# Kernel optimization log

Measured on AMD Instinct MI355X. Metric: run time of the kernel, lower is better.

## Reference

```python
import jax, jax.numpy as jnp
import numpy as np

B, D, E, K = 8192, 1024, 8, 5  # batch, in_dim, num_size_classes, num_depth_classes
H = max(64, D)                 # hidden = max(64, in_dim)
EPS = 1e-8


def ordinal_logits_to_probs(logits, num_classes):
    # logits: [B, K-1] cumulative ordinal logits -> [B, K] class probs
    q = jax.nn.sigmoid(logits)
    probs = jnp.concatenate(
        [1.0 - q[:, :1], q[:, :-1] - q[:, 1:], q[:, -1:]], axis=1
    )  # [B, K]
    probs = jnp.clip(probs, EPS)
    return probs / jnp.clip(probs.sum(axis=1, keepdims=True), EPS)


def setup_inputs() -> dict:
    key = jax.random.key(0)
    kx, ks, k1, k2 = jax.random.split(key, 4)
    x = jax.random.normal(kx, (B, D), dtype=jnp.float32)
    size_idx = jax.random.randint(ks, (B,), 0, E, dtype=jnp.int64)
    # per-expert 2-layer MLP params: Linear(D,H) -> ReLU -> Linear(H,K-1)
    W1 = jax.random.normal(k1, (E, D, H), dtype=jnp.float32) / np.sqrt(D)
    b1 = jnp.zeros((E, H), dtype=jnp.float32)
    W2 = jax.random.normal(k2, (E, H, K - 1), dtype=jnp.float32) / np.sqrt(H)
    b2 = jnp.zeros((E, K - 1), dtype=jnp.float32)
    return {"x": x, "size_idx": size_idx, "W1": W1, "b1": b1, "W2": W2, "b2": b2}


def reference(x, size_idx, W1, b1, W2, b2):
    # Hard routing: each token gets the output of expert size_idx[b].
    # Dense all-expert compute + per-token select (same math as mask/gather/scatter,
    # dropout is inference-mode identity).
    h = jax.nn.relu(jnp.einsum('bd,edh->beh', x, W1) + b1)      # [B, E, H]
    all_logits = jnp.einsum('beh,ehk->bek', h, W2) + b2          # [B, E, K-1]
    idx = size_idx.astype(jnp.int32)[:, None, None]              # [B, 1, 1]
    logits = jnp.take_along_axis(all_logits, idx, axis=1)[:, 0]  # [B, K-1]
    probs = ordinal_logits_to_probs(logits, K)                   # [B, K]
    return logits, probs
```

## Files before the change

kernel.cpp:

```cpp
#include <hip/hip_runtime.h>
#include <cstdint>
#include <cstddef>

#define Bn 8192
#define Dn 1024
#define Hn 1024
#define En 8
#define MT 128
#define MAX_TILES (Bn / MT + En)
#define PERM_N (Bn + En * MT)

typedef unsigned short u16;
typedef __bf16 bf16x8 __attribute__((ext_vector_type(8)));
typedef float f32x4 __attribute__((ext_vector_type(4)));
typedef unsigned short ushort8 __attribute__((ext_vector_type(8)));

__device__ __forceinline__ u16 f2bf(float f) {
  unsigned int u = __float_as_uint(f);
  unsigned int r = u + 0x7fffu + ((u >> 16) & 1u);
  return (u16)(r >> 16);
}

__device__ __forceinline__ void gld16(const void* g, void* l) {
  __builtin_amdgcn_global_load_lds(
      (const __attribute__((address_space(1))) void*)g,
      (__attribute__((address_space(3))) void*)l, 16, 0, 0);
}

__global__ __launch_bounds__(1024) void route_k(const int* __restrict__ sidx,
                                                int* __restrict__ off,
                                                int* __restrict__ perm) {
  __shared__ int hist[16][En];
  __shared__ int base[16][En];
  __shared__ int eoff[En + 1];
  int t = threadIdx.x;
  int wv = t >> 6;
  if (t < 16 * En) ((int*)hist)[t] = 0;
  __syncthreads();
  int e8[8], r8[8];
#pragma unroll
  for (int i = 0; i < 8; i++) {
    int e = sidx[t + i * 1024];
    e8[i] = e;
    r8[i] = atomicAdd(&hist[wv][e], 1);
  }
  __syncthreads();
  if (t < En) {
    int s = 0;
    for (int w = 0; w < 16; w++) { base[w][t] = s; s += hist[w][t]; }
    hist[0][t] = s;
  }
  __syncthreads();
  if (t == 0) {
    int o = 0;
    for (int e = 0; e < En; e++) {
      eoff[e] = o; off[e] = o;
      o += (hist[0][e] + MT - 1) & ~(MT - 1);
    }
    eoff[En] = o; off[En] = o;
  }
  __syncthreads();
#pragma unroll
  for (int i = 0; i < 8; i++) {
    int e = e8[i];
    perm[eoff[e] + base[wv][e] + r8[i]] = t + i * 1024;
  }
}

__global__ void cvt_x_k(const float* __restrict__ x, u16* __restrict__ xb) {
  size_t i = ((size_t)blockIdx.x * blockDim.x + threadIdx.x) * 8;
  float4 a = *(const float4*)(x + i);
  float4 b = *(const float4*)(x + i + 4);
  ushort8 o;
  o[0] = f2bf(a.x); o[1] = f2bf(a.y); o[2] = f2bf(a.z); o[3] = f2bf(a.w);
  o[4] = f2bf(b.x); o[5] = f2bf(b.y); o[6] = f2bf(b.z); o[7] = f2bf(b.w);
  *(ushort8*)(xb + i) = o;
}

__global__ __launch_bounds__(256) void cvt_w1_k(const float* __restrict__ W1,
                                                u16* __restrict__ W1t) {
  __shared__ float tile[64][65];
  int e = blockIdx.z;
  int k0 = blockIdx.y * 64;
  int n0 = blockIdx.x * 64;
  int c = threadIdx.x & 63, r0 = threadIdx.x >> 6;
  const float* src = W1 + ((size_t)e << 20) + (size_t)k0 * Hn + n0;
#pragma unroll
  for (int i = 0; i < 16; i++) {
    int r = r0 + i * 4;
    tile[r][c] = src[(size_t)r * Hn + c];
  }
  __syncthreads();
  u16* dst = W1t + ((size_t)e << 20) + (size_t)n0 * Dn + k0;
#pragma unroll
  for (int i = 0; i < 16; i++) {
    int h = r0 + i * 4;
    dst[(size_t)h * Dn + c] = f2bf(tile[c][h]);
  }
}

__global__ __launch_bounds__(256) void gemm_k(
    const u16* __restrict__ xb, const u16* __restrict__ w1t,
    const float* __restrict__ b1, const float* __restrict__ w2,
    const int* __restrict__ perm, const int* __restrict__ off,
    float* __restrict__ out) {
  __shared__ u16 As[2][128 * 32];
  __shared__ u16 Bs[2][128 * 32];

  int tb = blockIdx.x;
  int row0 = tb * MT;
  if (row0 >= off[En]) return;
  int e = 0;
  while (row0 >= off[e + 1]) e++;
  int n0 = blockIdx.y * 128;

  int tid = threadIdx.x;
  int lane = tid & 63, w = tid >> 6;
  int wm = w >> 1, wn = w & 1;

  int srow = lane >> 2;
  int slot = lane & 3;
  int q = slot ^ ((srow >> 1) & 3);
  int scol = q * 8;
  const u16* aG[2]; const u16* bG[2];
  u16* aL[2]; u16* bL[2];
#pragma unroll
  for (int j = 0; j < 2; j++) {
    int rl = 32 * w + 16 * j + srow;
    int tok = perm[row0 + rl];
    if (tok < 0) tok = 0;
    aG[j] = xb + (size_t)tok * Dn + scol;
    bG[j] = w1t + ((size_t)e << 20) + (size_t)(n0 + rl) * Dn + scol;
    aL[j] = (u16*)As + (32 * w + 16 * j) * 32;
    bL[j] = (u16*)Bs + (32 * w + 16 * j) * 32;
  }

  f32x4 acc[4][4];
#pragma unroll
  for (int i = 0; i < 4; i++)
#pragma unroll
    for (int j = 0; j < 4; j++)
      acc[i][j] = (f32x4){0.f, 0.f, 0.f, 0.f};

  int fr = lane & 15;
  int qf = lane >> 4;
  int sw = (fr >> 1) & 3;
  int offA[4], offB[4];
#pragma unroll
  for (int i = 0; i < 4; i++)
    offA[i] = (wm * 64 + i * 16 + fr) * 32 + (qf ^ sw) * 8;
#pragma unroll
  for (int j = 0; j < 4; j++)
    offB[j] = (wn * 64 + j * 16 + fr) * 32 + (qf ^ sw) * 8;

  gld16(aG[0], aL[0]); gld16(aG[1], aL[1]);
  gld16(bG[0], bL[0]); gld16(bG[1], bL[1]);

  int cur = 0;
  for (int k0 = 0; k0 < Dn; k0 += 32, cur ^= 1) {
    __syncthreads();
    if (k0 + 32 < Dn) {
      int nb = cur ^ 1;
      gld16(aG[0] + k0 + 32, aL[0] + nb * 4096);
      gld16(aG[1] + k0 + 32, aL[1] + nb * 4096);
      gld16(bG[0] + k0 + 32, bL[0] + nb * 4096);
      gld16(bG[1] + k0 + 32, bL[1] + nb * 4096);
    }
    const u16* Ab = (const u16*)As + cur * 4096;
    const u16* Bb = (const u16*)Bs + cur * 4096;
    bf16x8 af[4], bfr[4];
#pragma unroll
    for (int i = 0; i < 4; i++) af[i] = *(const bf16x8*)(Ab + offA[i]);
#pragma unroll
    for (int j = 0; j < 4; j++) bfr[j] = *(const bf16x8*)(Bb + offB[j]);
#pragma unroll
    for (int i = 0; i < 4; i++)
#pragma unroll
      for (int j = 0; j < 4; j++)
        acc[i][j] = __builtin_amdgcn_mfma_f32_16x16x32_bf16(af[i], bfr[j], acc[i][j], 0, 0, 0);
  }

  int fq = lane >> 4;
  float4 w2v[4]; float b1v[4];
#pragma unroll
  for (int j = 0; j < 4; j++) {
    int col = n0 + wn * 64 + j * 16 + fr;
    w2v[j] = *(const float4*)(w2 + ((size_t)e * Hn + col) * 4);
    b1v[j] = b1[(size_t)e * Hn + col];
  }
#pragma unroll
  for (int i = 0; i < 4; i++) {
    int rbase = wm * 64 + i * 16 + fq * 4;
#pragma unroll
    for (int r = 0; r < 4; r++) {
      float s0 = 0.f, s1 = 0.f, s2 = 0.f, s3 = 0.f;
#pragma unroll
      for (int j = 0; j < 4; j++) {
        float h = acc[i][j][r] + b1v[j];
        h = fmaxf(h, 0.f);
        s0 = fmaf(h, w2v[j].x, s0);
        s1 = fmaf(h, w2v[j].y, s1);
        s2 = fmaf(h, w2v[j].z, s2);
        s3 = fmaf(h, w2v[j].w, s3);
      }
#pragma unroll
      for (int m = 1; m < 16; m <<= 1) {
        s0 += __shfl_xor(s0, m);
        s1 += __shfl_xor(s1, m);
        s2 += __shfl_xor(s2, m);
        s3 += __shfl_xor(s3, m);
      }
      if (fr == 0) {
        int tok = perm[row0 + rbase + r];
        if (tok >= 0) {
          float* o = out + (size_t)tok * 4;
          atomicAdd(o + 0, s0);
          atomicAdd(o + 1, s1);
          atomicAdd(o + 2, s2);
          atomicAdd(o + 3, s3);
        }
      }
    }
  }
}

__global__ void probs_k(float* __restrict__ out, const float* __restrict__ b2,
                        const int* __restrict__ sidx) {
  int b = blockIdx.x * blockDim.x + threadIdx.x;
  if (b >= Bn) return;
  int e = sidx[b];
  float l0 = out[b * 4 + 0] + b2[e * 4 + 0];
  float l1 = out[b * 4 + 1] + b2[e * 4 + 1];
  float l2 = out[b * 4 + 2] + b2[e * 4 + 2];
  float l3 = out[b * 4 + 3] + b2[e * 4 + 3];
  out[b * 4 + 0] = l0; out[b * 4 + 1] = l1;
  out[b * 4 + 2] = l2; out[b * 4 + 3] = l3;
  float q0 = 1.f / (1.f + expf(-l0));
  float q1 = 1.f / (1.f + expf(-l1));
  float q2 = 1.f / (1.f + expf(-l2));
  float q3 = 1.f / (1.f + expf(-l3));
  const float eps = 1e-8f;
  float p0 = fmaxf(1.f - q0, eps);
  float p1 = fmaxf(q0 - q1, eps);
  float p2 = fmaxf(q1 - q2, eps);
  float p3 = fmaxf(q2 - q3, eps);
  float p4 = fmaxf(q3, eps);
  float s = p0 + p1 + p2 + p3 + p4;
  float inv = 1.f / fmaxf(s, eps);
  float* pr = out + (size_t)Bn * 4 + (size_t)b * 5;
  pr[0] = p0 * inv; pr[1] = p1 * inv; pr[2] = p2 * inv;
  pr[3] = p3 * inv; pr[4] = p4 * inv;
}

extern "C" void kernel_launch(void* const* d_in, const int* in_sizes, int n_in,
                              void* d_out, int out_size, void* d_ws, size_t ws_size,
                              hipStream_t stream) {
  const float* x  = (const float*)d_in[0];
  const int* sidx = (const int*)d_in[1];
  const float* W1 = (const float*)d_in[2];
  const float* b1 = (const float*)d_in[3];
  const float* W2 = (const float*)d_in[4];
  const float* b2 = (const float*)d_in[5];
  float* out = (float*)d_out;

  uint8_t* w = (uint8_t*)d_ws;
  int* off  = (int*)(w + 64);
  int* perm = (int*)(w + 512);
  u16* xb   = (u16*)(w + 40960);
  u16* w1t  = (u16*)(w + 40960 + (size_t)16777216);

  hipMemsetAsync(perm, 0xFF, PERM_N * sizeof(int), stream);
  hipMemsetAsync(d_out, 0, (size_t)Bn * 4 * sizeof(float), stream);

  route_k<<<1, 1024, 0, stream>>>(sidx, off, perm);
  cvt_x_k<<<(Bn * Dn) / (256 * 8), 256, 0, stream>>>(x, xb);
  cvt_w1_k<<<dim3(Hn / 64, Dn / 64, En), 256, 0, stream>>>(W1, w1t);
  gemm_k<<<dim3(MAX_TILES, Hn / 128), 256, 0, stream>>>(xb, w1t, b1, W2, perm, off, out);
  probs_k<<<Bn / 256, 256, 0, stream>>>(out, b2, sidx);
}
```

Measured before the change: 181.0 us.

## Pre-permute x into expert order, shrink GEMM N-tile, replace atomics with partials

The x conversion now gathers rows by the routing permutation, so the GEMM reads contiguous pre-sorted, zero-padded bf16 rows instead of indirect token rows. The GEMM N tile shrinks from 128 to 64, which doubles the grid for better occupancy. Each block writes per-row partial second-layer sums to a workspace buffer instead of doing float atomics. The probs kernel then reduces the 16 partials per row and scatters the results to token order. The W1 transpose-convert kernel is also vectorized with float4 loads and ushort4 stores. The cost is a partials buffer, a padded x copy, and lower reuse of the A tile per block.

```diff
diff --git a/kernel.cpp b/kernel.cpp
--- a/kernel.cpp
+++ b/kernel.cpp
@@ -7,6 +7,8 @@
 #define Hn 1024
 #define En 8
 #define MT 128
+#define NTILE 64
+#define NB (Hn / NTILE)
 #define MAX_TILES (Bn / MT + En)
 #define PERM_N (Bn + En * MT)
 
@@ -67,14 +69,24 @@
   }
 }
 
-__global__ void cvt_x_k(const float* __restrict__ x, u16* __restrict__ xb) {
-  size_t i = ((size_t)blockIdx.x * blockDim.x + threadIdx.x) * 8;
-  float4 a = *(const float4*)(x + i);
-  float4 b = *(const float4*)(x + i + 4);
+__global__ __launch_bounds__(256) void cvt_xp_k(const float* __restrict__ x,
+                                                const int* __restrict__ perm,
+                                                u16* __restrict__ xbp) {
+  size_t idx = ((size_t)blockIdx.x * 256 + threadIdx.x) * 8;
+  int p = (int)(idx >> 10);
+  int col = (int)(idx & 1023);
+  int tok = perm[p];
   ushort8 o;
-  o[0] = f2bf(a.x); o[1] = f2bf(a.y); o[2] = f2bf(a.z); o[3] = f2bf(a.w);
-  o[4] = f2bf(b.x); o[5] = f2bf(b.y); o[6] = f2bf(b.z); o[7] = f2bf(b.w);
-  *(ushort8*)(xb + i) = o;
+  if (tok < 0) {
+    o = (ushort8){0, 0, 0, 0, 0, 0, 0, 0};
+  } else {
+    const float* src = x + ((size_t)tok << 10) + col;
+    float4 a = *(const float4*)src;
+    float4 b = *(const float4*)(src + 4);
+    o[0] = f2bf(a.x); o[1] = f2bf(a.y); o[2] = f2bf(a.z); o[3] = f2bf(a.w);
+    o[4] = f2bf(b.x); o[5] = f2bf(b.y); o[6] = f2bf(b.z); o[7] = f2bf(b.w);
+  }
+  *(ushort8*)(xbp + idx) = o;
 }
 
 __global__ __launch_bounds__(256) void cvt_w1_k(const float* __restrict__ W1,
@@ -83,78 +95,77 @@
   int e = blockIdx.z;
   int k0 = blockIdx.y * 64;
   int n0 = blockIdx.x * 64;
-  int c = threadIdx.x & 63, r0 = threadIdx.x >> 6;
+  int c4 = (threadIdx.x & 15) * 4;
+  int r0 = threadIdx.x >> 4;
   const float* src = W1 + ((size_t)e << 20) + (size_t)k0 * Hn + n0;
 #pragma unroll
-  for (int i = 0; i < 16; i++) {
-    int r = r0 + i * 4;
-    tile[r][c] = src[(size_t)r * Hn + c];
+  for (int i = 0; i < 4; i++) {
+    int r = r0 + i * 16;
+    float4 v = *(const float4*)(src + (size_t)r * Hn + c4);
+    tile[r][c4 + 0] = v.x; tile[r][c4 + 1] = v.y;
+    tile[r][c4 + 2] = v.z; tile[r][c4 + 3] = v.w;
   }
   __syncthreads();
   u16* dst = W1t + ((size_t)e << 20) + (size_t)n0 * Dn + k0;
 #pragma unroll
-  for (int i = 0; i < 16; i++) {
-    int h = r0 + i * 4;
-    dst[(size_t)h * Dn + c] = f2bf(tile[c][h]);
+  for (int i = 0; i < 4; i++) {
+    int h = r0 + i * 16;
+    ushort4 o;
+    o.x = f2bf(tile[c4 + 0][h]);
+    o.y = f2bf(tile[c4 + 1][h]);
+    o.z = f2bf(tile[c4 + 2][h]);
+    o.w = f2bf(tile[c4 + 3][h]);
+    *(ushort4*)(dst + (size_t)h * Dn + c4) = o;
   }
 }
 
 __global__ __launch_bounds__(256) void gemm_k(
-    const u16* __restrict__ xb, const u16* __restrict__ w1t,
+    const u16* __restrict__ xbp, const u16* __restrict__ w1t,
     const float* __restrict__ b1, const float* __restrict__ w2,
-    const int* __restrict__ perm, const int* __restrict__ off,
-    float* __restrict__ out) {
+    const int* __restrict__ off, float* __restrict__ partials) {
   __shared__ u16 As[2][128 * 32];
-  __shared__ u16 Bs[2][128 * 32];
+  __shared__ u16 Bs[2][64 * 32];
 
   int tb = blockIdx.x;
   int row0 = tb * MT;
   if (row0 >= off[En]) return;
   int e = 0;
   while (row0 >= off[e + 1]) e++;
-  int n0 = blockIdx.y * 128;
+  int n0 = blockIdx.y * NTILE;
 
   int tid = threadIdx.x;
   int lane = tid & 63, w = tid >> 6;
-  int wm = w >> 1, wn = w & 1;
 
   int srow = lane >> 2;
   int slot = lane & 3;
-  int q = slot ^ ((srow >> 1) & 3);
-  int scol = q * 8;
-  const u16* aG[2]; const u16* bG[2];
-  u16* aL[2]; u16* bL[2];
+  int scol = (slot ^ ((srow >> 1) & 3)) * 8;
+  const u16* aG[2]; u16* aL[2];
 #pragma unroll
   for (int j = 0; j < 2; j++) {
     int rl = 32 * w + 16 * j + srow;
-    int tok = perm[row0 + rl];
-    if (tok < 0) tok = 0;
-    aG[j] = xb + (size_t)tok * Dn + scol;
-    bG[j] = w1t + ((size_t)e << 20) + (size_t)(n0 + rl) * Dn + scol;
+    aG[j] = xbp + (size_t)(row0 + rl) * Dn + scol;
     aL[j] = (u16*)As + (32 * w + 16 * j) * 32;
-    bL[j] = (u16*)Bs + (32 * w + 16 * j) * 32;
-  }
-
-  f32x4 acc[4][4];
-#pragma unroll
-  for (int i = 0; i < 4; i++)
+  }
+  const u16* bG = w1t + ((size_t)e << 20) + (size_t)(n0 + 16 * w + srow) * Dn + scol;
+  u16* bL = (u16*)Bs + (16 * w) * 32;
+
+  f32x4 acc[2][4];
+#pragma unroll
+  for (int i = 0; i < 2; i++)
 #pragma unroll
     for (int j = 0; j < 4; j++)
       acc[i][j] = (f32x4){0.f, 0.f, 0.f, 0.f};
 
   int fr = lane & 15;
   int qf = lane >> 4;
-  int sw = (fr >> 1) & 3;
-  int offA[4], offB[4];
-#pragma unroll
-  for (int i = 0; i < 4; i++)
-    offA[i] = (wm * 64 + i * 16 + fr) * 32 + (qf ^ sw) * 8;
-#pragma unroll
-  for (int j = 0; j < 4; j++)
-    offB[j] = (wn * 64 + j * 16 + fr) * 32 + (qf ^ sw) * 8;
-
-  gld16(aG[0], aL[0]); gld16(aG[1], aL[1]);
-  gld16(bG[0], bL[0]); gld16(bG[1], bL[1]);
+  int qs = (qf ^ ((fr >> 1) & 3)) * 8;
+  int offA[2], offB[4];
+#pragma unroll
+  for (int i = 0; i < 2; i++) offA[i] = (w * 32 + i * 16 + fr) * 32 + qs;
+#pragma unroll
+  for (int j = 0; j < 4; j++) offB[j] = (j * 16 + fr) * 32 + qs;
+
+  gld16(aG[0], aL[0]); gld16(aG[1], aL[1]); gld16(bG, bL);
 
   int cur = 0;
   for (int k0 = 0; k0 < Dn; k0 += 32, cur ^= 1) {
@@ -163,34 +174,31 @@
       int nb = cur ^ 1;
       gld16(aG[0] + k0 + 32, aL[0] + nb * 4096);
       gld16(aG[1] + k0 + 32, aL[1] + nb * 4096);
-      gld16(bG[0] + k0 + 32, bL[0] + nb * 4096);
-      gld16(bG[1] + k0 + 32, bL[1] + nb * 4096);
+      gld16(bG + k0 + 32, bL + nb * 2048);
     }
     const u16* Ab = (const u16*)As + cur * 4096;
-    const u16* Bb = (const u16*)Bs + cur * 4096;
-    bf16x8 af[4], bfr[4];
-#pragma unroll
-    for (int i = 0; i < 4; i++) af[i] = *(const bf16x8*)(Ab + offA[i]);
+    const u16* Bb = (const u16*)Bs + cur * 2048;
+    bf16x8 af[2], bfr[4];
+#pragma unroll
+    for (int i = 0; i < 2; i++) af[i] = *(const bf16x8*)(Ab + offA[i]);
 #pragma unroll
     for (int j = 0; j < 4; j++) bfr[j] = *(const bf16x8*)(Bb + offB[j]);
 #pragma unroll
-    for (int i = 0; i < 4; i++)
+    for (int i = 0; i < 2; i++)
 #pragma unroll
       for (int j = 0; j < 4; j++)
         acc[i][j] = __builtin_amdgcn_mfma_f32_16x16x32_bf16(af[i], bfr[j], acc[i][j], 0, 0, 0);
   }
 
-  int fq = lane >> 4;
   float4 w2v[4]; float b1v[4];
 #pragma unroll
   for (int j = 0; j < 4; j++) {
-    int col = n0 + wn * 64 + j * 16 + fr;
+    int col = n0 + j * 16 + fr;
     w2v[j] = *(const float4*)(w2 + ((size_t)e * Hn + col) * 4);
     b1v[j] = b1[(size_t)e * Hn + col];
   }
 #pragma unroll
-  for (int i = 0; i < 4; i++) {
-    int rbase = wm * 64 + i * 16 + fq * 4;
+  for (int i = 0; i < 2; i++) {
 #pragma unroll
     for (int r = 0; r < 4; r++) {
       float s0 = 0.f, s1 = 0.f, s2 = 0.f, s3 = 0.f;
@@ -211,30 +219,35 @@
         s3 += __shfl_xor(s3, m);
       }
       if (fr == 0) {
-        int tok = perm[row0 + rbase + r];
-        if (tok >= 0) {
-          float* o = out + (size_t)tok * 4;
-          atomicAdd(o + 0, s0);
-          atomicAdd(o + 1, s1);
-          atomicAdd(o + 2, s2);
-          atomicAdd(o + 3, s3);
-        }
+        int row = w * 32 + i * 16 + qf * 4 + r;
+        *(float4*)(partials + ((size_t)(row0 + row) * NB + blockIdx.y) * 4) =
+            make_float4(s0, s1, s2, s3);
       }
     }
   }
 }
 
-__global__ void probs_k(float* __restrict__ out, const float* __restrict__ b2,
-                        const int* __restrict__ sidx) {
-  int b = blockIdx.x * blockDim.x + threadIdx.x;
-  if (b >= Bn) return;
-  int e = sidx[b];
-  float l0 = out[b * 4 + 0] + b2[e * 4 + 0];
-  float l1 = out[b * 4 + 1] + b2[e * 4 + 1];
-  float l2 = out[b * 4 + 2] + b2[e * 4 + 2];
-  float l3 = out[b * 4 + 3] + b2[e * 4 + 3];
-  out[b * 4 + 0] = l0; out[b * 4 + 1] = l1;
-  out[b * 4 + 2] = l2; out[b * 4 + 3] = l3;
+__global__ void probs_k(const float* __restrict__ partials,
+                        const int* __restrict__ perm, const int* __restrict__ off,
+                        const int* __restrict__ sidx, const float* __restrict__ b2,
+                        float* __restrict__ out) {
+  int p = blockIdx.x * blockDim.x + threadIdx.x;
+  if (p >= off[En]) return;
+  int tok = perm[p];
+  if (tok < 0) return;
+  int e = sidx[tok];
+  float s0 = 0.f, s1 = 0.f, s2 = 0.f, s3 = 0.f;
+#pragma unroll
+  for (int nb = 0; nb < NB; nb++) {
+    float4 v = *(const float4*)(partials + ((size_t)p * NB + nb) * 4);
+    s0 += v.x; s1 += v.y; s2 += v.z; s3 += v.w;
+  }
+  float l0 = s0 + b2[e * 4 + 0];
+  float l1 = s1 + b2[e * 4 + 1];
+  float l2 = s2 + b2[e * 4 + 2];
+  float l3 = s3 + b2[e * 4 + 3];
+  out[tok * 4 + 0] = l0; out[tok * 4 + 1] = l1;
+  out[tok * 4 + 2] = l2; out[tok * 4 + 3] = l3;
   float q0 = 1.f / (1.f + expf(-l0));
   float q1 = 1.f / (1.f + expf(-l1));
   float q2 = 1.f / (1.f + expf(-l2));
@@ -247,7 +260,7 @@
   float p4 = fmaxf(q3, eps);
   float s = p0 + p1 + p2 + p3 + p4;
   float inv = 1.f / fmaxf(s, eps);
-  float* pr = out + (size_t)Bn * 4 + (size_t)b * 5;
+  float* pr = out + (size_t)Bn * 4 + (size_t)tok * 5;
   pr[0] = p0 * inv; pr[1] = p1 * inv; pr[2] = p2 * inv;
   pr[3] = p3 * inv; pr[4] = p4 * inv;
 }
@@ -266,15 +279,15 @@
   uint8_t* w = (uint8_t*)d_ws;
   int* off  = (int*)(w + 64);
   int* perm = (int*)(w + 512);
-  u16* xb   = (u16*)(w + 40960);
-  u16* w1t  = (u16*)(w + 40960 + (size_t)16777216);
+  u16* xbp      = (u16*)(w + 40960);
+  u16* w1t      = (u16*)(w + 18919424);
+  float* parts  = (float*)(w + 35700736);
 
   hipMemsetAsync(perm, 0xFF, PERM_N * sizeof(int), stream);
-  hipMemsetAsync(d_out, 0, (size_t)Bn * 4 * sizeof(float), stream);
 
   route_k<<<1, 1024, 0, stream>>>(sidx, off, perm);
-  cvt_x_k<<<(Bn * Dn) / (256 * 8), 256, 0, stream>>>(x, xb);
+  cvt_xp_k<<<(PERM_N * Dn) / (256 * 8), 256, 0, stream>>>(x, perm, xbp);
   cvt_w1_k<<<dim3(Hn / 64, Dn / 64, En), 256, 0, stream>>>(W1, w1t);
-  gemm_k<<<dim3(MAX_TILES, Hn / 128), 256, 0, stream>>>(xb, w1t, b1, W2, perm, off, out);
-  probs_k<<<Bn / 256, 256, 0, stream>>>(out, b2, sidx);
-}
+  gemm_k<<<dim3(MAX_TILES, NB), 256, 0, stream>>>(xbp, w1t, b1, W2, off, parts);
+  probs_k<<<(PERM_N + 255) / 256, 256, 0, stream>>>(parts, perm, off, sidx, b2, out);
+}
```

Result: faster. 174.7 us (-3.5%).
